# Kernel tuning notes

Measured on AMD Instinct MI355X. Metric: run time of the kernel, lower is better.

Reference implementation:

```python
import jax, jax.numpy as jnp
import numpy as np


def _safe_norm(x, eps=1e-8):
    return jnp.sqrt(jnp.clip(jnp.sum(x * x, axis=-1, keepdims=True), eps))


def _normalize(x, eps=1e-8):
    return x / _safe_norm(x, eps)


def _safe_direction(primary, fallback, eps=1e-6):
    bad = _safe_norm(primary, eps) < eps  # [N,1] bool
    out = jnp.where(bad, fallback, primary)
    return _normalize(out, eps)


def _build_frames(x):
    # x: [N,3] (N >= 2). Returns per-node rotation frames [N,3,3] (columns = axes).
    d = x[1:] - x[:-1]
    prev = jnp.concatenate([d[:1], d], axis=0)
    nxt = jnp.concatenate([d, d[-1:]], axis=0)
    tangent = _safe_direction(prev + nxt, nxt)
    curvature = _safe_direction(nxt - prev, prev)
    ay_raw = curvature - tangent * jnp.sum(curvature * tangent, axis=-1, keepdims=True)
    ay = _safe_direction(ay_raw, jnp.cross(tangent, prev))
    az = _safe_direction(jnp.cross(tangent, ay), jnp.cross(tangent, curvature))
    ay = _safe_direction(jnp.cross(az, tangent), ay)
    return jnp.stack([tangent, ay, az], axis=-1)


def setup_inputs() -> dict:
    key = jax.random.key(0)
    N, H, EH = 1024, 256, 128  # EH = max(16, H//2)
    ks = jax.random.split(key, 16)

    def lin(k, fi, fo):
        k1, k2 = jax.random.split(k)
        lim = 1.0 / np.sqrt(fi)
        W = jax.random.uniform(k1, (fi, fo), minval=-lim, maxval=lim, dtype=jnp.float32)
        b = jax.random.uniform(k2, (fo,), minval=-lim, maxval=lim, dtype=jnp.float32)
        return W, b

    h = jax.random.normal(ks[0], (N, H), dtype=jnp.float32)
    x_cond = jnp.cumsum(jax.random.normal(ks[1], (N, 3), dtype=jnp.float32) * 1.5, axis=0)
    x_t = x_cond + 0.05 * jax.random.normal(ks[2], (N, 3), dtype=jnp.float32)
    tau = jax.random.uniform(ks[3], (1,), dtype=jnp.float32)
    W_np1, b_np1 = lin(ks[4], H + 6, H)
    W_np2, b_np2 = lin(ks[5], H, H)
    w_src, b_src = lin(ks[6], H, 1)
    w_dst, b_dst = lin(ks[7], H, 1)
    w_ns, b_ns = lin(ks[8], H, 1)
    W_eg1, b_eg1 = lin(ks[9], 4, EH)
    w_eg2, b_eg2 = lin(ks[10], EH, 1)
    W_out1, b_out1 = lin(ks[11], H + 6, H)
    W_out2, b_out2 = lin(ks[12], H, 3)
    return dict(h=h, x_t=x_t, x_cond=x_cond, tau=tau,
                W_np1=W_np1, b_np1=b_np1, W_np2=W_np2, b_np2=b_np2,
                w_src=w_src, b_src=b_src, w_dst=w_dst, b_dst=b_dst,
                w_ns=w_ns, b_ns=b_ns, W_eg1=W_eg1, b_eg1=b_eg1,
                w_eg2=w_eg2, b_eg2=b_eg2, W_out1=W_out1, b_out1=b_out1,
                W_out2=W_out2, b_out2=b_out2)


def reference(h, x_t, x_cond, tau,
              W_np1, b_np1, W_np2, b_np2,
              w_src, b_src, w_dst, b_dst,
              w_ns, b_ns, W_eg1, b_eg1, w_eg2, b_eg2,
              W_out1, b_out1, W_out2, b_out2):
    silu = jax.nn.silu
    n = x_t.shape[0]
    frames = _build_frames(x_cond)                       # [N,3,3]
    delta = x_t - x_cond
    delta_local = jnp.einsum('nji,nj->ni', frames, delta)  # frames^T @ delta
    t = tau.reshape(())
    t_emb = jnp.broadcast_to(jnp.stack([t, jnp.sin(t), jnp.cos(t)]), (n, 3))
    node_feat = jnp.concatenate([h, delta_local, t_emb], axis=-1)
    nh = silu(node_feat @ W_np1 + b_np1)
    nh = silu(nh @ W_np2 + b_np2)                        # [N,H]
    # pairwise local geometry: rel[n,m] = x[m] - x[n], rotated into node n's frame
    rel = x_t[None, :, :] - x_t[:, None, :]              # [N,N,3]
    rel_local = jnp.einsum('nji,nmj->nmi', frames, rel)  # [N,N,3]
    dist = jnp.linalg.norm(rel_local, axis=-1, keepdims=True)
    edge_feat = jnp.concatenate([rel_local, dist], axis=-1)  # [N,N,4]
    eh = silu(edge_feat @ W_eg1 + b_eg1)                 # [N,N,EH]
    edge_logit = (eh @ w_eg2 + b_eg2)[..., 0]            # [N,N]
    src = nh @ w_src + b_src                             # [N,1] -> broadcast over m
    dst = (nh @ w_dst + b_dst)[:, 0]                     # [N]
    logits = src + dst[None, :] + edge_logit             # [N,N]
    diag = jnp.eye(n, dtype=bool)
    logits = jnp.where(diag, -10000.0, logits)
    attn = jax.nn.softmax(logits, axis=1)
    attn = jnp.where(diag, 0.0, attn)
    attn = attn / jnp.clip(jnp.sum(attn, axis=1, keepdims=True), 1e-6)
    ns = jax.nn.sigmoid(nh @ w_ns + b_ns)[:, 0]          # [N]
    msgs = jnp.einsum('nm,m,nmi->ni', attn, ns, rel_local)  # [N,3]
    uf = jnp.concatenate([nh, delta_local, msgs], axis=-1)
    local_update = silu(uf @ W_out1 + b_out1) @ W_out2 + b_out2
    vel_local = local_update + 0.25 * msgs
    return jnp.einsum('nij,nj->ni', frames, vel_local)
```

## Files before the change

### kernel.cpp

```cpp
#include <hip/hip_runtime.h>
#include <math.h>

#define DEV __device__ __forceinline__

struct F3 { float x, y, z; };

DEV F3 mkf3(float x, float y, float z){ F3 r; r.x=x; r.y=y; r.z=z; return r; }
DEV F3 f3add(F3 a, F3 b){ return mkf3(a.x+b.x, a.y+b.y, a.z+b.z); }
DEV F3 f3sub(F3 a, F3 b){ return mkf3(a.x-b.x, a.y-b.y, a.z-b.z); }
DEV F3 f3scale(F3 a, float s){ return mkf3(a.x*s, a.y*s, a.z*s); }
DEV float f3dot(F3 a, F3 b){ return a.x*b.x + a.y*b.y + a.z*b.z; }
DEV F3 f3cross(F3 a, F3 b){
  return mkf3(a.y*b.z - a.z*b.y, a.z*b.x - a.x*b.z, a.x*b.y - a.y*b.x);
}
DEV F3 f3dir(F3 v){
  float ss = f3dot(v, v);
  float inv = 1.0f / sqrtf(fmaxf(ss, 1e-6f));
  return f3scale(v, inv);
}
DEV float fast_silu(float x){
  return x * __builtin_amdgcn_rcpf(1.0f + __expf(-x));
}
DEV float fast_sigmoid(float x){
  return __builtin_amdgcn_rcpf(1.0f + __expf(-x));
}

__global__ void frames_kernel(const float* __restrict__ xc,
                              const float* __restrict__ xt,
                              float* __restrict__ frames,
                              float* __restrict__ dl, int N)
{
  int n = blockIdx.x * blockDim.x + threadIdx.x;
  if (n >= N) return;
  int pn = (n > 0) ? n - 1 : 0;
  int qn = (n < N - 1) ? n : N - 2;
  F3 prev = mkf3(xc[(pn+1)*3+0]-xc[pn*3+0], xc[(pn+1)*3+1]-xc[pn*3+1], xc[(pn+1)*3+2]-xc[pn*3+2]);
  F3 nxt  = mkf3(xc[(qn+1)*3+0]-xc[qn*3+0], xc[(qn+1)*3+1]-xc[qn*3+1], xc[(qn+1)*3+2]-xc[qn*3+2]);

  F3 tangent = f3dir(f3add(prev, nxt));
  F3 curv    = f3dir(f3sub(nxt, prev));
  float ct   = f3dot(curv, tangent);
  F3 ay      = f3dir(f3sub(curv, f3scale(tangent, ct)));
  F3 az      = f3dir(f3cross(tangent, ay));
  ay         = f3dir(f3cross(az, tangent));

  float* fr = frames + n * 9;
  fr[0] = tangent.x; fr[1] = ay.x; fr[2] = az.x;
  fr[3] = tangent.y; fr[4] = ay.y; fr[5] = az.y;
  fr[6] = tangent.z; fr[7] = ay.z; fr[8] = az.z;

  F3 delta = mkf3(xt[n*3+0]-xc[n*3+0], xt[n*3+1]-xc[n*3+1], xt[n*3+2]-xc[n*3+2]);
  dl[n*3+0] = f3dot(tangent, delta);
  dl[n*3+1] = f3dot(ay, delta);
  dl[n*3+2] = f3dot(az, delta);
}

__global__ __launch_bounds__(256) void node_mlp1(
    const float* __restrict__ h, const float* __restrict__ dl,
    const float* __restrict__ tau,
    const float* __restrict__ W1, const float* __restrict__ b1,
    float* __restrict__ nh1, int N)
{
  const int n0 = blockIdx.x * 4, tid = threadIdx.x;
  __shared__ float4 feat4[262];
  {
    const float* hp = h + n0 * 256 + tid;
    feat4[tid] = make_float4(hp[0], hp[256], hp[512], hp[768]);
  }
  if (tid < 6) {
    int k = 256 + tid;
    float4 v;
    if (tid < 3) {
      v = make_float4(dl[(n0+0)*3+tid], dl[(n0+1)*3+tid],
                      dl[(n0+2)*3+tid], dl[(n0+3)*3+tid]);
    } else {
      float t = tau[0];
      float s = (tid == 3) ? t : ((tid == 4) ? sinf(t) : cosf(t));
      v = make_float4(s, s, s, s);
    }
    feat4[k] = v;
  }
  __syncthreads();

  float bb = b1[tid];
  float a0 = bb, a1 = bb, a2 = bb, a3 = bb;
  const float* Wp = W1 + tid;
  for (int kb = 0; kb < 256; kb += 64) {
    float w[64];
    #pragma unroll
    for (int u = 0; u < 64; ++u) w[u] = Wp[(kb + u) * 256];
    #pragma unroll
    for (int u = 0; u < 64; ++u) {
      float4 f = feat4[kb + u];
      a0 = fmaf(f.x, w[u], a0); a1 = fmaf(f.y, w[u], a1);
      a2 = fmaf(f.z, w[u], a2); a3 = fmaf(f.w, w[u], a3);
    }
  }
  #pragma unroll
  for (int k = 256; k < 262; ++k) {
    float w = Wp[k * 256];
    float4 f = feat4[k];
    a0 = fmaf(f.x, w, a0); a1 = fmaf(f.y, w, a1);
    a2 = fmaf(f.z, w, a2); a3 = fmaf(f.w, w, a3);
  }
  nh1[(n0+0)*256+tid] = fast_silu(a0);
  nh1[(n0+1)*256+tid] = fast_silu(a1);
  nh1[(n0+2)*256+tid] = fast_silu(a2);
  nh1[(n0+3)*256+tid] = fast_silu(a3);
}

__global__ __launch_bounds__(256) void node_mlp2(
    const float* __restrict__ nh1,
    const float* __restrict__ W2, const float* __restrict__ b2,
    const float* __restrict__ w_src, const float* __restrict__ b_src,
    const float* __restrict__ w_dst, const float* __restrict__ b_dst,
    const float* __restrict__ w_ns, const float* __restrict__ b_ns,
    float* __restrict__ nh, float* __restrict__ srcv,
    float* __restrict__ dstv, float* __restrict__ nsv, int N)
{
  const int n0 = blockIdx.x * 4, tid = threadIdx.x;
  __shared__ float4 feat4[256];
  __shared__ float red[4][4][3];
  {
    const float* hp = nh1 + n0 * 256 + tid;
    feat4[tid] = make_float4(hp[0], hp[256], hp[512], hp[768]);
  }
  __syncthreads();

  float bb = b2[tid];
  float a0 = bb, a1 = bb, a2 = bb, a3 = bb;
  const float* Wp = W2 + tid;
  for (int kb = 0; kb < 256; kb += 64) {
    float w[64];
    #pragma unroll
    for (int u = 0; u < 64; ++u) w[u] = Wp[(kb + u) * 256];
    #pragma unroll
    for (int u = 0; u < 64; ++u) {
      float4 f = feat4[kb + u];
      a0 = fmaf(f.x, w[u], a0); a1 = fmaf(f.y, w[u], a1);
      a2 = fmaf(f.z, w[u], a2); a3 = fmaf(f.w, w[u], a3);
    }
  }

  const float wsv = w_src[tid], wdv = w_dst[tid], wnv = w_ns[tid];
  const int wave = tid >> 6, lane = tid & 63;
  float va[4] = {fast_silu(a0), fast_silu(a1), fast_silu(a2), fast_silu(a3)};
  #pragma unroll
  for (int r = 0; r < 4; ++r) {
    nh[(n0 + r) * 256 + tid] = va[r];
    float ps = va[r] * wsv, pd = va[r] * wdv, pn = va[r] * wnv;
    for (int off = 32; off; off >>= 1) {
      ps += __shfl_down(ps, off);
      pd += __shfl_down(pd, off);
      pn += __shfl_down(pn, off);
    }
    if (lane == 0) { red[wave][r][0] = ps; red[wave][r][1] = pd; red[wave][r][2] = pn; }
  }
  __syncthreads();
  if (tid < 4) {
    int r = tid;
    float s0 = 0.f, s1 = 0.f, s2 = 0.f;
    #pragma unroll
    for (int w = 0; w < 4; ++w) { s0 += red[w][r][0]; s1 += red[w][r][1]; s2 += red[w][r][2]; }
    srcv[n0 + r] = s0 + b_src[0];
    dstv[n0 + r] = s1 + b_dst[0];
    nsv[n0 + r]  = fast_sigmoid(s2 + b_ns[0]);
  }
}

__global__ __launch_bounds__(512, 8) void edge_softmax(
    const float* __restrict__ x_t, const float* __restrict__ frames,
    const float* __restrict__ srcv, const float* __restrict__ dstv,
    const float* __restrict__ nsv,
    const float* __restrict__ W_eg1, const float* __restrict__ b_eg1,
    const float* __restrict__ w_eg2, const float* __restrict__ b_eg2,
    float* __restrict__ msgs, int N)
{
  const int n = blockIdx.x, tid = threadIdx.x;
  __shared__ float4 wA[128];
  __shared__ float2 wB[128];
  __shared__ float frs[9], xns[3], srcs_;
  __shared__ float redmax[8];
  __shared__ float red[8][4];

  if (tid < 128) {
    const float nl2e = -1.44269504088896340736f;
    const float nln2 = -0.69314718055994530942f;
    wA[tid] = make_float4(nl2e * W_eg1[tid], nl2e * W_eg1[128 + tid],
                          nl2e * W_eg1[256 + tid], nl2e * W_eg1[384 + tid]);
    wB[tid] = make_float2(nl2e * b_eg1[tid], nln2 * w_eg2[tid]);
  }
  if (tid < 9) frs[tid] = frames[n * 9 + tid];
  if (tid < 3) xns[tid] = x_t[n * 3 + tid];
  if (tid == 0) srcs_ = srcv[n];
  __syncthreads();

  const float f0 = frs[0], f1 = frs[1], f2 = frs[2],
              f3_ = frs[3], f4 = frs[4], f5 = frs[5],
              f6 = frs[6], f7 = frs[7], f8 = frs[8];
  const float x0 = xns[0], x1 = xns[1], x2 = xns[2];
  const float sn = srcs_;
  const float b2v = b_eg2[0];

  float l[2], r0[2], r1[2], r2[2];
  float lmax = -3.4e38f;

  #pragma unroll
  for (int mi = 0; mi < 2; ++mi) {
    const int m = mi * 512 + tid;
    float rx = x_t[m * 3 + 0] - x0;
    float ry = x_t[m * 3 + 1] - x1;
    float rz = x_t[m * 3 + 2] - x2;
    float rl0 = f0 * rx + f3_ * ry + f6 * rz;
    float rl1 = f1 * rx + f4 * ry + f7 * rz;
    float rl2 = f2 * rx + f5 * ry + f8 * rz;
    float dist = sqrtf(rl0 * rl0 + rl1 * rl1 + rl2 * rl2);
    float acc = b2v;
    #pragma unroll 8
    for (int j = 0; j < 128; ++j) {
      float4 w = wA[j];
      float2 v = wB[j];
      float tp = fmaf(w.x, rl0, fmaf(w.y, rl1, fmaf(w.z, rl2, fmaf(w.w, dist, v.x))));
      float e  = __builtin_amdgcn_exp2f(tp);
      float sg = __builtin_amdgcn_rcpf(1.0f + e);
      acc = fmaf(v.y, tp * sg, acc);
    }
    float lg = sn + dstv[m] + acc;
    if (m == n) lg = -10000.0f;
    l[mi] = lg; r0[mi] = rl0; r1[mi] = rl1; r2[mi] = rl2;
    lmax = fmaxf(lmax, lg);
  }

  for (int off = 32; off; off >>= 1) lmax = fmaxf(lmax, __shfl_down(lmax, off));
  const int wave = tid >> 6, lane = tid & 63;
  if (lane == 0) redmax[wave] = lmax;
  __syncthreads();
  float mx = redmax[0];
  #pragma unroll
  for (int w = 1; w < 8; ++w) mx = fmaxf(mx, redmax[w]);

  float sum = 0.f, a0 = 0.f, a1 = 0.f, a2 = 0.f;
  #pragma unroll
  for (int mi = 0; mi < 2; ++mi) {
    const int m = mi * 512 + tid;
    float e = __expf(l[mi] - mx);
    sum += e;
    float w = e * nsv[m];
    a0 = fmaf(w, r0[mi], a0);
    a1 = fmaf(w, r1[mi], a1);
    a2 = fmaf(w, r2[mi], a2);
  }
  for (int off = 32; off; off >>= 1) {
    sum += __shfl_down(sum, off);
    a0 += __shfl_down(a0, off);
    a1 += __shfl_down(a1, off);
    a2 += __shfl_down(a2, off);
  }
  if (lane == 0) { red[wave][0] = sum; red[wave][1] = a0; red[wave][2] = a1; red[wave][3] = a2; }
  __syncthreads();
  if (tid == 0) {
    float Z = 0.f, m0 = 0.f, m1 = 0.f, m2 = 0.f;
    #pragma unroll
    for (int w = 0; w < 8; ++w) {
      Z += red[w][0]; m0 += red[w][1]; m1 += red[w][2]; m2 += red[w][3];
    }
    float invZ = 1.0f / Z;
    msgs[n * 3 + 0] = m0 * invZ;
    msgs[n * 3 + 1] = m1 * invZ;
    msgs[n * 3 + 2] = m2 * invZ;
  }
}

__global__ __launch_bounds__(256) void out_mlp(
    const float* __restrict__ nh, const float* __restrict__ dl,
    const float* __restrict__ msgs, const float* __restrict__ frames,
    const float* __restrict__ W1, const float* __restrict__ b1,
    const float* __restrict__ W2, const float* __restrict__ b2,
    float* __restrict__ out, int N)
{
  const int n0 = blockIdx.x * 4, tid = threadIdx.x;
  __shared__ float4 feat4[262];
  __shared__ float red[4][4][3];
  {
    const float* hp = nh + n0 * 256 + tid;
    feat4[tid] = make_float4(hp[0], hp[256], hp[512], hp[768]);
  }
  if (tid < 6) {
    int k = 256 + tid;
    float4 v;
    if (tid < 3) {
      v = make_float4(dl[(n0+0)*3+tid], dl[(n0+1)*3+tid],
                      dl[(n0+2)*3+tid], dl[(n0+3)*3+tid]);
    } else {
      int c = tid - 3;
      v = make_float4(msgs[(n0+0)*3+c], msgs[(n0+1)*3+c],
                      msgs[(n0+2)*3+c], msgs[(n0+3)*3+c]);
    }
    feat4[k] = v;
  }
  __syncthreads();

  float bb = b1[tid];
  float a0 = bb, a1 = bb, a2 = bb, a3 = bb;
  const float* Wp = W1 + tid;
  for (int kb = 0; kb < 256; kb += 64) {
    float w[64];
    #pragma unroll
    for (int u = 0; u < 64; ++u) w[u] = Wp[(kb + u) * 256];
    #pragma unroll
    for (int u = 0; u < 64; ++u) {
      float4 f = feat4[kb + u];
      a0 = fmaf(f.x, w[u], a0); a1 = fmaf(f.y, w[u], a1);
      a2 = fmaf(f.z, w[u], a2); a3 = fmaf(f.w, w[u], a3);
    }
  }
  #pragma unroll
  for (int k = 256; k < 262; ++k) {
    float w = Wp[k * 256];
    float4 f = feat4[k];
    a0 = fmaf(f.x, w, a0); a1 = fmaf(f.y, w, a1);
    a2 = fmaf(f.z, w, a2); a3 = fmaf(f.w, w, a3);
  }

  const float w0 = W2[tid * 3 + 0], w1 = W2[tid * 3 + 1], w2 = W2[tid * 3 + 2];
  const int wave = tid >> 6, lane = tid & 63;
  float va[4] = {fast_silu(a0), fast_silu(a1), fast_silu(a2), fast_silu(a3)};
  #pragma unroll
  for (int r = 0; r < 4; ++r) {
    float p0 = va[r] * w0, p1 = va[r] * w1, p2 = va[r] * w2;
    for (int off = 32; off; off >>= 1) {
      p0 += __shfl_down(p0, off);
      p1 += __shfl_down(p1, off);
      p2 += __shfl_down(p2, off);
    }
    if (lane == 0) { red[wave][r][0] = p0; red[wave][r][1] = p1; red[wave][r][2] = p2; }
  }
  __syncthreads();
  if (tid < 4) {
    int r = tid, n = n0 + r;
    float s0 = 0.f, s1 = 0.f, s2 = 0.f;
    #pragma unroll
    for (int w = 0; w < 4; ++w) { s0 += red[w][r][0]; s1 += red[w][r][1]; s2 += red[w][r][2]; }
    float m0 = msgs[n * 3 + 0], m1 = msgs[n * 3 + 1], m2 = msgs[n * 3 + 2];
    float v0 = s0 + b2[0] + 0.25f * m0;
    float v1 = s1 + b2[1] + 0.25f * m1;
    float v2 = s2 + b2[2] + 0.25f * m2;
    const float* fr = frames + n * 9;
    out[n * 3 + 0] = fr[0] * v0 + fr[1] * v1 + fr[2] * v2;
    out[n * 3 + 1] = fr[3] * v0 + fr[4] * v1 + fr[5] * v2;
    out[n * 3 + 2] = fr[6] * v0 + fr[7] * v1 + fr[8] * v2;
  }
}

extern "C" void kernel_launch(void* const* d_in, const int* in_sizes, int n_in,
                              void* d_out, int out_size, void* d_ws, size_t ws_size,
                              hipStream_t stream) {
  const float* h      = (const float*)d_in[0];
  const float* x_t    = (const float*)d_in[1];
  const float* x_cond = (const float*)d_in[2];
  const float* tau    = (const float*)d_in[3];
  const float* W_np1  = (const float*)d_in[4];
  const float* b_np1  = (const float*)d_in[5];
  const float* W_np2  = (const float*)d_in[6];
  const float* b_np2  = (const float*)d_in[7];
  const float* w_src  = (const float*)d_in[8];
  const float* b_src  = (const float*)d_in[9];
  const float* w_dst  = (const float*)d_in[10];
  const float* b_dst  = (const float*)d_in[11];
  const float* w_ns   = (const float*)d_in[12];
  const float* b_ns   = (const float*)d_in[13];
  const float* W_eg1  = (const float*)d_in[14];
  const float* b_eg1  = (const float*)d_in[15];
  const float* w_eg2  = (const float*)d_in[16];
  const float* b_eg2  = (const float*)d_in[17];
  const float* W_out1 = (const float*)d_in[18];
  const float* b_out1 = (const float*)d_in[19];
  const float* W_out2 = (const float*)d_in[20];
  const float* b_out2 = (const float*)d_in[21];
  float* out = (float*)d_out;

  const int N = in_sizes[1] / 3;

  float* ws     = (float*)d_ws;
  float* frames = ws;
  float* dl     = frames + N * 9;
  float* nh1    = dl + N * 3;
  float* nh     = nh1 + N * 256;
  float* srcv   = nh + N * 256;
  float* dstv   = srcv + N;
  float* nsv    = dstv + N;
  float* msgs   = nsv + N;

  frames_kernel<<<(N + 255) / 256, 256, 0, stream>>>(x_cond, x_t, frames, dl, N);
  node_mlp1<<<N / 4, 256, 0, stream>>>(h, dl, tau, W_np1, b_np1, nh1, N);
  node_mlp2<<<N / 4, 256, 0, stream>>>(nh1, W_np2, b_np2, w_src, b_src,
                                       w_dst, b_dst, w_ns, b_ns,
                                       nh, srcv, dstv, nsv, N);
  edge_softmax<<<N, 512, 0, stream>>>(x_t, frames, srcv, dstv, nsv,
                                      W_eg1, b_eg1, w_eg2, b_eg2, msgs, N);
  out_mlp<<<N / 4, 256, 0, stream>>>(nh, dl, msgs, frames,
                                     W_out1, b_out1, W_out2, b_out2, out, N);
}
```

Measured before the change: 75.38 us.

## Fuse node MLP kernels and split edge hidden units across lanes in softmax

The two node MLP layers are merged into one kernel, so the first layer's activations stay in shared memory instead of making a global round trip, and one launch is saved. The edge softmax kernel now stages relative positions, dst/ns values and logits in shared memory. Each group of 16 lanes holds 8 hidden-unit weights in registers and reduces the per-edge logit with xor shuffles, where before each thread looped over all 128 hidden units reading weights from LDS. This raises LDS use (about 28KB per block) and lowers the occupancy hint from 8 to 4, and it adds shuffle-reduction cost in exchange for fewer LDS weight reads.

```diff
diff --git a/kernel.cpp b/kernel.cpp
--- a/kernel.cpp
+++ b/kernel.cpp
@@ -55,17 +55,25 @@
   dl[n*3+2] = f3dot(az, delta);
 }
 
-__global__ __launch_bounds__(256) void node_mlp1(
+__global__ __launch_bounds__(256) void node_mlp(
     const float* __restrict__ h, const float* __restrict__ dl,
     const float* __restrict__ tau,
     const float* __restrict__ W1, const float* __restrict__ b1,
-    float* __restrict__ nh1, int N)
+    const float* __restrict__ W2, const float* __restrict__ b2,
+    const float* __restrict__ w_src, const float* __restrict__ b_src,
+    const float* __restrict__ w_dst, const float* __restrict__ b_dst,
+    const float* __restrict__ w_ns, const float* __restrict__ b_ns,
+    float* __restrict__ nh, float* __restrict__ srcv,
+    float* __restrict__ dstv, float* __restrict__ nsv, int N)
 {
   const int n0 = blockIdx.x * 4, tid = threadIdx.x;
-  __shared__ float4 feat4[262];
+  __shared__ float4 fA[262];
+  __shared__ float4 fB[256];
+  __shared__ float red[4][4][3];
+
   {
     const float* hp = h + n0 * 256 + tid;
-    feat4[tid] = make_float4(hp[0], hp[256], hp[512], hp[768]);
+    fA[tid] = make_float4(hp[0], hp[256], hp[512], hp[768]);
   }
   if (tid < 6) {
     int k = 256 + tid;
@@ -78,52 +86,33 @@
       float s = (tid == 3) ? t : ((tid == 4) ? sinf(t) : cosf(t));
       v = make_float4(s, s, s, s);
     }
-    feat4[k] = v;
-  }
-  __syncthreads();
-
-  float bb = b1[tid];
-  float a0 = bb, a1 = bb, a2 = bb, a3 = bb;
-  const float* Wp = W1 + tid;
-  for (int kb = 0; kb < 256; kb += 64) {
-    float w[64];
-    #pragma unroll
-    for (int u = 0; u < 64; ++u) w[u] = Wp[(kb + u) * 256];
-    #pragma unroll
-    for (int u = 0; u < 64; ++u) {
-      float4 f = feat4[kb + u];
-      a0 = fmaf(f.x, w[u], a0); a1 = fmaf(f.y, w[u], a1);
-      a2 = fmaf(f.z, w[u], a2); a3 = fmaf(f.w, w[u], a3);
-    }
-  }
-  #pragma unroll
-  for (int k = 256; k < 262; ++k) {
-    float w = Wp[k * 256];
-    float4 f = feat4[k];
-    a0 = fmaf(f.x, w, a0); a1 = fmaf(f.y, w, a1);
-    a2 = fmaf(f.z, w, a2); a3 = fmaf(f.w, w, a3);
-  }
-  nh1[(n0+0)*256+tid] = fast_silu(a0);
-  nh1[(n0+1)*256+tid] = fast_silu(a1);
-  nh1[(n0+2)*256+tid] = fast_silu(a2);
-  nh1[(n0+3)*256+tid] = fast_silu(a3);
-}
-
-__global__ __launch_bounds__(256) void node_mlp2(
-    const float* __restrict__ nh1,
-    const float* __restrict__ W2, const float* __restrict__ b2,
-    const float* __restrict__ w_src, const float* __restrict__ b_src,
-    const float* __restrict__ w_dst, const float* __restrict__ b_dst,
-    const float* __restrict__ w_ns, const float* __restrict__ b_ns,
-    float* __restrict__ nh, float* __restrict__ srcv,
-    float* __restrict__ dstv, float* __restrict__ nsv, int N)
-{
-  const int n0 = blockIdx.x * 4, tid = threadIdx.x;
-  __shared__ float4 feat4[256];
-  __shared__ float red[4][4][3];
+    fA[k] = v;
+  }
+  __syncthreads();
+
   {
-    const float* hp = nh1 + n0 * 256 + tid;
-    feat4[tid] = make_float4(hp[0], hp[256], hp[512], hp[768]);
+    float bb = b1[tid];
+    float a0 = bb, a1 = bb, a2 = bb, a3 = bb;
+    const float* Wp = W1 + tid;
+    for (int kb = 0; kb < 256; kb += 64) {
+      float w[64];
+      #pragma unroll
+      for (int u = 0; u < 64; ++u) w[u] = Wp[(kb + u) * 256];
+      #pragma unroll
+      for (int u = 0; u < 64; ++u) {
+        float4 f = fA[kb + u];
+        a0 = fmaf(f.x, w[u], a0); a1 = fmaf(f.y, w[u], a1);
+        a2 = fmaf(f.z, w[u], a2); a3 = fmaf(f.w, w[u], a3);
+      }
+    }
+    #pragma unroll
+    for (int k = 256; k < 262; ++k) {
+      float w = Wp[k * 256];
+      float4 f = fA[k];
+      a0 = fmaf(f.x, w, a0); a1 = fmaf(f.y, w, a1);
+      a2 = fmaf(f.z, w, a2); a3 = fmaf(f.w, w, a3);
+    }
+    fB[tid] = make_float4(fast_silu(a0), fast_silu(a1), fast_silu(a2), fast_silu(a3));
   }
   __syncthreads();
 
@@ -136,7 +125,7 @@
     for (int u = 0; u < 64; ++u) w[u] = Wp[(kb + u) * 256];
     #pragma unroll
     for (int u = 0; u < 64; ++u) {
-      float4 f = feat4[kb + u];
+      float4 f = fB[kb + u];
       a0 = fmaf(f.x, w[u], a0); a1 = fmaf(f.y, w[u], a1);
       a2 = fmaf(f.z, w[u], a2); a3 = fmaf(f.w, w[u], a3);
     }
@@ -168,7 +157,7 @@
   }
 }
 
-__global__ __launch_bounds__(512, 8) void edge_softmax(
+__global__ __launch_bounds__(512, 4) void edge_softmax(
     const float* __restrict__ x_t, const float* __restrict__ frames,
     const float* __restrict__ srcv, const float* __restrict__ dstv,
     const float* __restrict__ nsv,
@@ -177,33 +166,18 @@
     float* __restrict__ msgs, int N)
 {
   const int n = blockIdx.x, tid = threadIdx.x;
-  __shared__ float4 wA[128];
-  __shared__ float2 wB[128];
-  __shared__ float frs[9], xns[3], srcs_;
-  __shared__ float redmax[8];
-  __shared__ float red[8][4];
-
-  if (tid < 128) {
-    const float nl2e = -1.44269504088896340736f;
-    const float nln2 = -0.69314718055994530942f;
-    wA[tid] = make_float4(nl2e * W_eg1[tid], nl2e * W_eg1[128 + tid],
-                          nl2e * W_eg1[256 + tid], nl2e * W_eg1[384 + tid]);
-    wB[tid] = make_float2(nl2e * b_eg1[tid], nln2 * w_eg2[tid]);
-  }
-  if (tid < 9) frs[tid] = frames[n * 9 + tid];
-  if (tid < 3) xns[tid] = x_t[n * 3 + tid];
-  if (tid == 0) srcs_ = srcv[n];
-  __syncthreads();
-
-  const float f0 = frs[0], f1 = frs[1], f2 = frs[2],
-              f3_ = frs[3], f4 = frs[4], f5 = frs[5],
-              f6 = frs[6], f7 = frs[7], f8 = frs[8];
-  const float x0 = xns[0], x1 = xns[1], x2 = xns[2];
-  const float sn = srcs_;
+  __shared__ float4 rel4[1024];
+  __shared__ float2 dn[1024];
+  __shared__ float  l_s[1024];
+  __shared__ float  redmax[8];
+  __shared__ float  red[8][4];
+
+  const float f0 = frames[n*9+0], f1 = frames[n*9+1], f2 = frames[n*9+2],
+              f3_ = frames[n*9+3], f4 = frames[n*9+4], f5 = frames[n*9+5],
+              f6 = frames[n*9+6], f7 = frames[n*9+7], f8 = frames[n*9+8];
+  const float x0 = x_t[n*3+0], x1 = x_t[n*3+1], x2 = x_t[n*3+2];
+  const float sn = srcv[n];
   const float b2v = b_eg2[0];
-
-  float l[2], r0[2], r1[2], r2[2];
-  float lmax = -3.4e38f;
 
   #pragma unroll
   for (int mi = 0; mi < 2; ++mi) {
@@ -215,24 +189,50 @@
     float rl1 = f1 * rx + f4 * ry + f7 * rz;
     float rl2 = f2 * rx + f5 * ry + f8 * rz;
     float dist = sqrtf(rl0 * rl0 + rl1 * rl1 + rl2 * rl2);
-    float acc = b2v;
-    #pragma unroll 8
-    for (int j = 0; j < 128; ++j) {
-      float4 w = wA[j];
-      float2 v = wB[j];
-      float tp = fmaf(w.x, rl0, fmaf(w.y, rl1, fmaf(w.z, rl2, fmaf(w.w, dist, v.x))));
+    rel4[m] = make_float4(rl0, rl1, rl2, dist);
+    dn[m]   = make_float2(dstv[m], nsv[m]);
+  }
+
+  const int lane = tid & 63, wave = tid >> 6;
+  const int jsub = lane & 15;
+  const float nl2e = -1.44269504088896340736f;
+  const float nln2 = -0.69314718055994530942f;
+  float w0r[8], w1r[8], w2r[8], w3r[8], wbr[8], w2o[8];
+  #pragma unroll
+  for (int u = 0; u < 8; ++u) {
+    int j = u * 16 + jsub;
+    w0r[u] = nl2e * W_eg1[j];
+    w1r[u] = nl2e * W_eg1[128 + j];
+    w2r[u] = nl2e * W_eg1[256 + j];
+    w3r[u] = nl2e * W_eg1[384 + j];
+    wbr[u] = nl2e * b_eg1[j];
+    w2o[u] = nln2 * w_eg2[j];
+  }
+  __syncthreads();
+
+  float lmax = -3.4e38f;
+  const int grp = lane >> 4;
+  for (int i = 0; i < 32; ++i) {
+    const int m = wave * 128 + i * 4 + grp;
+    float4 rd = rel4[m];
+    float acc = 0.f;
+    #pragma unroll
+    for (int u = 0; u < 8; ++u) {
+      float tp = fmaf(w0r[u], rd.x, fmaf(w1r[u], rd.y,
+                 fmaf(w2r[u], rd.z, fmaf(w3r[u], rd.w, wbr[u]))));
       float e  = __builtin_amdgcn_exp2f(tp);
       float sg = __builtin_amdgcn_rcpf(1.0f + e);
-      acc = fmaf(v.y, tp * sg, acc);
-    }
-    float lg = sn + dstv[m] + acc;
+      acc = fmaf(w2o[u], tp * sg, acc);
+    }
+    #pragma unroll
+    for (int mask = 1; mask < 16; mask <<= 1) acc += __shfl_xor(acc, mask);
+    float lg = sn + dn[m].x + b2v + acc;
     if (m == n) lg = -10000.0f;
-    l[mi] = lg; r0[mi] = rl0; r1[mi] = rl1; r2[mi] = rl2;
     lmax = fmaxf(lmax, lg);
+    if (jsub == 0) l_s[m] = lg;
   }
 
   for (int off = 32; off; off >>= 1) lmax = fmaxf(lmax, __shfl_down(lmax, off));
-  const int wave = tid >> 6, lane = tid & 63;
   if (lane == 0) redmax[wave] = lmax;
   __syncthreads();
   float mx = redmax[0];
@@ -243,12 +243,13 @@
   #pragma unroll
   for (int mi = 0; mi < 2; ++mi) {
     const int m = mi * 512 + tid;
-    float e = __expf(l[mi] - mx);
+    float4 rd = rel4[m];
+    float e = __expf(l_s[m] - mx);
     sum += e;
-    float w = e * nsv[m];
-    a0 = fmaf(w, r0[mi], a0);
-    a1 = fmaf(w, r1[mi], a1);
-    a2 = fmaf(w, r2[mi], a2);
+    float w = e * dn[m].y;
+    a0 = fmaf(w, rd.x, a0);
+    a1 = fmaf(w, rd.y, a1);
+    a2 = fmaf(w, rd.z, a2);
   }
   for (int off = 32; off; off >>= 1) {
     sum += __shfl_down(sum, off);
@@ -384,18 +385,16 @@
   float* ws     = (float*)d_ws;
   float* frames = ws;
   float* dl     = frames + N * 9;
-  float* nh1    = dl + N * 3;
-  float* nh     = nh1 + N * 256;
+  float* nh     = dl + N * 3;
   float* srcv   = nh + N * 256;
   float* dstv   = srcv + N;
   float* nsv    = dstv + N;
   float* msgs   = nsv + N;
 
   frames_kernel<<<(N + 255) / 256, 256, 0, stream>>>(x_cond, x_t, frames, dl, N);
-  node_mlp1<<<N / 4, 256, 0, stream>>>(h, dl, tau, W_np1, b_np1, nh1, N);
-  node_mlp2<<<N / 4, 256, 0, stream>>>(nh1, W_np2, b_np2, w_src, b_src,
-                                       w_dst, b_dst, w_ns, b_ns,
-                                       nh, srcv, dstv, nsv, N);
+  node_mlp<<<N / 4, 256, 0, stream>>>(h, dl, tau, W_np1, b_np1, W_np2, b_np2,
+                                      w_src, b_src, w_dst, b_dst, w_ns, b_ns,
+                                      nh, srcv, dstv, nsv, N);
   edge_softmax<<<N, 512, 0, stream>>>(x_t, frames, srcv, dstv, nsv,
                                       W_eg1, b_eg1, w_eg2, b_eg2, msgs, N);
   out_mlp<<<N / 4, 256, 0, stream>>>(nh, dl, msgs, frames,
```

New measurement: 82.77 us. 1.1x slower.
